# Optimization experiments

Measured on AMD Instinct MI355X. Metric: run time of the kernel, lower is better.

The kernel has to match this reference:

```python
import jax, jax.numpy as jnp
import numpy as np


def setup_inputs() -> dict:
    key = jax.random.key(0)
    ks = jax.random.split(key, 4)
    B, S, D, V = 2, 2048, 768, 50257
    scale = 1.0 / np.sqrt(D)
    x = jax.random.normal(ks[0], (B, S, D), dtype=jnp.float32)
    W_vocab = jax.random.normal(ks[1], (V, D), dtype=jnp.float32) * scale
    b_vocab = jnp.zeros((V,), dtype=jnp.float32)
    W_lin = jax.random.normal(ks[2], (D, D), dtype=jnp.float32) * scale
    b_lin = jnp.zeros((D,), dtype=jnp.float32)
    return {"x": x, "W_vocab": W_vocab, "b_vocab": b_vocab, "W_lin": W_lin, "b_lin": b_lin}


def reference(x, W_vocab, b_vocab, W_lin, b_lin):
    # vocab_attention_layer(x): [B,S,D] @ [D,V] + b -> [B,S,V]
    logits = jnp.einsum('bsd,vd->bsv', x, W_vocab) + b_vocab
    va = jax.nn.softmax(logits, axis=-1)                      # [B,S,V]
    # einsum('bij,jk->bik', va, weight): contract vocab against embedding rows
    va_weight = jnp.einsum('bsv,vd->bsd', va, W_vocab)        # [B,S,D]
    # final nn.Linear(d_model, d_model): y = h @ W^T + b
    return jnp.einsum('bsd,ed->bse', va_weight, W_lin) + b_lin
```

## Files before the change

### kernel.cpp

```cpp
#include <hip/hip_runtime.h>
#include <hip/hip_bf16.h>
#include <stdint.h>

typedef float f32x4 __attribute__((ext_vector_type(4)));
typedef short s16x8 __attribute__((ext_vector_type(8)));
typedef unsigned short u16;

#define M_ROWS 4096
#define DIM    768
#define VOCAB  50257
#define VP2    50432

#define OFF_XB     0ull
#define OFF_WLB    6291456ull
#define OFF_WVB    7471104ull
#define OFF_WVT    84934656ull
#define OFF_P      162398208ull
#define OFF_ORUN   229507072ull
#define OFF_LROW   242089984ull
#define OFF_BROW   242106368ull
#define OFF_KEYS   242122752ull
#define OFF_H      242122880ull

__device__ __forceinline__ u16 f2bf(float f) {
    union { float f; unsigned u; } x; x.f = f;
    return (u16)((x.u + 0x7fffu + ((x.u >> 16) & 1u)) >> 16);
}
__device__ __forceinline__ float bf2f_hi(unsigned u) {
    union { unsigned u; float f; } x; x.u = u & 0xffff0000u; return x.f;
}
__device__ __forceinline__ float bf2f_lo(unsigned u) {
    union { unsigned u; float f; } x; x.u = u << 16; return x.f;
}
__device__ __forceinline__ unsigned fkey(float f) {
    union { float f; unsigned u; } x; x.f = f;
    return (x.u & 0x80000000u) ? ~x.u : (x.u | 0x80000000u);
}
__device__ __forceinline__ float fkey_dec(unsigned k) {
    union { unsigned u; float f; } x;
    x.u = (k & 0x80000000u) ? (k & 0x7fffffffu) : ~k;
    return x.f;
}
__device__ __forceinline__ void glds16(const u16* g, u16* l) {
    __builtin_amdgcn_global_load_lds(
        (const __attribute__((address_space(1))) unsigned int*)g,
        (__attribute__((address_space(3))) unsigned int*)l,
        16, 0, 0);
}

__global__ __launch_bounds__(256) void cast_bf16(const float* __restrict__ src,
                                                 u16* __restrict__ dst, int n4) {
    int i = blockIdx.x * 256 + threadIdx.x;
    if (i >= n4) return;
    float4 v = ((const float4*)src)[i];
    ushort4 o;
    o.x = f2bf(v.x); o.y = f2bf(v.y); o.z = f2bf(v.z); o.w = f2bf(v.w);
    ((ushort4*)dst)[i] = o;
}

__global__ __launch_bounds__(256) void prep_wvb(const float* __restrict__ wv,
                                                u16* __restrict__ wvb, int ntask) {
    int t = blockIdx.x * 256 + threadIdx.x;
    if (t >= ntask) return;
    int v = t / 96, ch = t % 96;
    uint4 pk = {0u, 0u, 0u, 0u};
    if (v < VOCAB) {
        const float* p = wv + (size_t)v * DIM + ch * 8;
        float4 f0 = ((const float4*)p)[0];
        float4 f1 = ((const float4*)p)[1];
        pk.x = (unsigned)f2bf(f0.x) | ((unsigned)f2bf(f0.y) << 16);
        pk.y = (unsigned)f2bf(f0.z) | ((unsigned)f2bf(f0.w) << 16);
        pk.z = (unsigned)f2bf(f1.x) | ((unsigned)f2bf(f1.y) << 16);
        pk.w = (unsigned)f2bf(f1.z) | ((unsigned)f2bf(f1.w) << 16);
    }
    *(uint4*)(wvb + (size_t)v * DIM + ch * 8) = pk;
}

__global__ void init_keys(unsigned* keys) {
    keys[0] = 0u;
    keys[1] = fkey(-3.0e38f);
}

__global__ __launch_bounds__(256) void wnorm(const u16* __restrict__ wvb,
                                             unsigned* __restrict__ keys) {
    __shared__ float part[128];
    int tid = threadIdx.x;
    int vb = blockIdx.x * 32;
    int vl = tid & 31, cg = tid >> 5;
    float s = 0.f;
    #pragma unroll
    for (int it = 0; it < 12; ++it) {
        int ch = cg + 8 * it;
        uint4 pk = *(const uint4*)(wvb + (size_t)(vb + vl) * DIM + ch * 8);
        const unsigned* pw = (const unsigned*)&pk;
        #pragma unroll
        for (int k = 0; k < 4; ++k) {
            float lo = bf2f_lo(pw[k]), hi = bf2f_hi(pw[k]);
            s += lo * lo + hi * hi;
        }
    }
    s += __shfl_xor(s, 32);
    int w = tid >> 6, lane = tid & 63;
    if (lane < 32) part[w * 32 + lane] = s;
    __syncthreads();
    if (tid < 32) {
        float t = part[tid] + part[32 + tid] + part[64 + tid] + part[96 + tid];
        float n = sqrtf(t);
        #pragma unroll
        for (int msk = 1; msk < 32; msk <<= 1) n = fmaxf(n, __shfl_xor(n, msk));
        if (tid == 0) atomicMax(&keys[0], __float_as_uint(n));
    }
}

__global__ __launch_bounds__(256) void bmax_k(const float* __restrict__ bv,
                                              unsigned* __restrict__ keys) {
    int i = blockIdx.x * 256 + threadIdx.x;
    float v = (i < VOCAB) ? bv[i] : -3.0e38f;
    #pragma unroll
    for (int msk = 1; msk < 64; msk <<= 1) v = fmaxf(v, __shfl_xor(v, msk));
    if ((threadIdx.x & 63) == 0) atomicMax(&keys[1], fkey(v));
}

__global__ __launch_bounds__(256) void xnorm(const float* __restrict__ x,
                                             const unsigned* __restrict__ keys,
                                             float* __restrict__ Brow) {
    int w = threadIdx.x >> 6, lane = threadIdx.x & 63;
    int r = blockIdx.x * 4 + w;
    const float4* p = (const float4*)(x + (size_t)r * DIM);
    float s = 0.f;
    #pragma unroll
    for (int it = 0; it < 3; ++it) {
        float4 v = p[it * 64 + lane];
        s += v.x * v.x + v.y * v.y + v.z * v.z + v.w * v.w;
    }
    #pragma unroll
    for (int msk = 1; msk < 64; msk <<= 1) s += __shfl_xor(s, msk);
    if (lane == 0) {
        float Wn = __uint_as_float(keys[0]);
        float bm = fkey_dec(keys[1]);
        Brow[r] = sqrtf(s) * Wn * 1.01f + bm + 0.1f;
    }
}

__global__ __launch_bounds__(256) void prep_wvt(const u16* __restrict__ wvb,
                                                u16* __restrict__ wvt) {
    __shared__ u16 tile[32][776];
    int vb = blockIdx.x * 32;
    int tid = threadIdx.x;
    #pragma unroll
    for (int it = 0; it < 12; ++it) {
        int task = tid + 256 * it;
        int row = task / 96, ch = task % 96;
        *(uint4*)(&tile[row][ch * 8]) = *(const uint4*)(wvb + (size_t)(vb + row) * DIM + ch * 8);
    }
    __syncthreads();
    #pragma unroll
    for (int it = 0; it < 12; ++it) {
        int task = tid + 256 * it;
        int d = task >> 2, vg = task & 3;
        u16 t8[8];
        #pragma unroll
        for (int j = 0; j < 8; ++j) t8[j] = tile[vg * 8 + j][d];
        uint4 pk;
        pk.x = (unsigned)t8[0] | ((unsigned)t8[1] << 16);
        pk.y = (unsigned)t8[2] | ((unsigned)t8[3] << 16);
        pk.z = (unsigned)t8[4] | ((unsigned)t8[5] << 16);
        pk.w = (unsigned)t8[6] | ((unsigned)t8[7] << 16);
        *(uint4*)(wvt + (size_t)d * VP2 + vb + vg * 8) = pk;
    }
}


template<int MH, int NH>
__device__ __forceinline__ void mfma_quad(f32x4 (&acc)[8][4],
                                          const s16x8 (&afr)[4][2],
                                          const s16x8 (&bfr)[2][2][2]) {
    #pragma unroll
    for (int mi = 0; mi < 4; ++mi)
        #pragma unroll
        for (int ni = 0; ni < 2; ++ni) {
            f32x4 a_ = acc[MH * 4 + mi][NH * 2 + ni];
            a_ = __builtin_amdgcn_mfma_f32_16x16x32_bf16(afr[mi][0], bfr[NH][ni][0], a_, 0, 0, 0);
            a_ = __builtin_amdgcn_mfma_f32_16x16x32_bf16(afr[mi][1], bfr[NH][ni][1], a_, 0, 0, 0);
            acc[MH * 4 + mi][NH * 2 + ni] = a_;
        }
}

#define STG(g, pitch, rowbase, kcol, ldst) do {                                   \
    const u16* _s0 = (g) + (size_t)((rowbase) + rlo) * (pitch) + (kcol) + offu;   \
    const u16* _s1 = _s0 + (size_t)64 * (pitch);                                  \
    glds16(_s0, (u16*)(ldst) + (size_t)tid * 8);                                  \
    glds16(_s1, (u16*)(ldst) + (size_t)tid * 8 + 4096);                           \
} while (0)

#define RD_A(buf, mh) do { _Pragma("unroll")                                              \
    for (int _mi = 0; _mi < 4; ++_mi) {                                                   \
        afr[_mi][0] = *(const s16x8*)((buf) + ((abase + ((mh)*4 + _mi)*2048)      ^ asw));\
        afr[_mi][1] = *(const s16x8*)((buf) + ((abase + ((mh)*4 + _mi)*2048 + 64) ^ asw));\
    } } while (0)

#define RD_B(buf, nh) do { _Pragma("unroll")                                              \
    for (int _ni = 0; _ni < 2; ++_ni) {                                                   \
        bfr[nh][_ni][0] = *(const s16x8*)((buf) + ((bbase + ((nh)*2 + _ni)*2048)      ^ asw));\
        bfr[nh][_ni][1] = *(const s16x8*)((buf) + ((bbase + ((nh)*2 + _ni)*2048 + 64) ^ asw));\
    } } while (0)

#define PH_SYNC1() do { __builtin_amdgcn_s_barrier();                      \
    asm volatile("s_waitcnt lgkmcnt(0)" ::: "memory");                     \
    __builtin_amdgcn_s_setprio(1); } while (0)
#define PH_SYNC2() do { __builtin_amdgcn_s_setprio(0);                     \
    __builtin_amdgcn_s_barrier(); } while (0)

__device__ __forceinline__ void kloop256(char* LDS,
                                         const u16* __restrict__ gA, int pA,
                                         const u16* __restrict__ gB, int pB,
                                         int NT, int tid, f32x4 (&acc)[8][4]) {
    const int lane = tid & 63, w = tid >> 6;
    const int c = lane & 15, q = (lane >> 4) & 3;
    const int wm = w & 1, wn = w >> 1;
    const int asw = (c & 7) << 4;
    const int abase = wm * 16384 + c * 128 + q * 16;
    const int bbase = (wn >> 1) * 16384 + (wn & 1) * 8192 + c * 128 + q * 16;
    const int rlo = tid >> 3;
    const int offu = ((tid & 7) * 8) ^ ((rlo & 7) << 3);
    char* A0 = LDS;
    char* B0 = LDS + 32768;
    char* A1 = LDS + 65536;
    char* B1 = LDS + 98304;
    s16x8 afr[4][2], bfr[2][2][2];
    const int ktN = NT - 1;

    STG(gA, pA, 0,   0, A0);
    STG(gA, pA, 128, 0, A0 + 16384);
    STG(gB, pB, 0,   0, B0);
    STG(gB, pB, 128, 0, B0 + 16384);
    {
        int k1 = (ktN >= 1 ? 1 : 0) * 64;
        STG(gB, pB, 0,   k1, B1);
        STG(gB, pB, 128, k1, B1 + 16384);
        STG(gA, pA, 0,   k1, A1);
    }
    asm volatile("s_waitcnt vmcnt(6)" ::: "memory");
    __builtin_amdgcn_s_barrier();

    const int nit = NT >> 1;
    #pragma unroll 1
    for (int it2 = 0; it2 < nit; ++it2) {
        int kO  = ((2 * it2 + 1 < NT) ? 2 * it2 + 1 : ktN) * 64;
        int kN0 = ((2 * it2 + 2 < NT) ? 2 * it2 + 2 : ktN) * 64;
        int kN1 = ((2 * it2 + 3 < NT) ? 2 * it2 + 3 : ktN) * 64;
        RD_A(A0, 0); RD_B(B0, 0);
        STG(gA, pA, 128, kO, A1 + 16384);
        PH_SYNC1(); mfma_quad<0, 0>(acc, afr, bfr); PH_SYNC2();
        RD_B(B0, 1);
        PH_SYNC1(); mfma_quad<0, 1>(acc, afr, bfr); PH_SYNC2();
        RD_A(A0, 1);
        STG(gB, pB, 0, kN0, B0);
        PH_SYNC1(); mfma_quad<1, 0>(acc, afr, bfr); PH_SYNC2();
        STG(gB, pB, 128, kN0, B0 + 16384);
        STG(gA, pA, 0,   kN0, A0);
        asm volatile("s_waitcnt vmcnt(6)" ::: "memory");
        PH_SYNC1(); mfma_quad<1, 1>(acc, afr, bfr); PH_SYNC2();
        RD_A(A1, 0); RD_B(B1, 0);
        STG(gA, pA, 128, kN0, A0 + 16384);
        PH_SYNC1(); mfma_quad<0, 0>(acc, afr, bfr); PH_SYNC2();
        RD_B(B1, 1);
        PH_SYNC1(); mfma_quad<0, 1>(acc, afr, bfr); PH_SYNC2();
        RD_A(A1, 1);
        STG(gB, pB, 0, kN1, B1);
        PH_SYNC1(); mfma_quad<1, 0>(acc, afr, bfr); PH_SYNC2();
        STG(gB, pB, 128, kN1, B1 + 16384);
        STG(gA, pA, 0,   kN1, A1);
        asm volatile("s_waitcnt vmcnt(6)" ::: "memory");
        PH_SYNC1(); mfma_quad<1, 1>(acc, afr, bfr); PH_SYNC2();
    }
}

__global__ __launch_bounds__(512, 2) void gemm1(
    const u16* __restrict__ xb, const u16* __restrict__ wvb,
    const float* __restrict__ bvocab, const float* __restrict__ Brow,
    u16* __restrict__ P, float* __restrict__ Lrow, int v0, int CN) {
    __shared__ __align__(16) char LDS[131072];
    __shared__ float BL[256];
    int tid = threadIdx.x;
    int mt = blockIdx.x & 15, nt = blockIdx.x >> 4;
    if (tid < 256) BL[tid] = Brow[mt * 256 + tid];
    f32x4 acc[8][4];
    #pragma unroll
    for (int i = 0; i < 8; ++i)
        #pragma unroll
        for (int j = 0; j < 4; ++j) acc[i][j] = (f32x4){0.f, 0.f, 0.f, 0.f};
    kloop256(LDS, xb + (size_t)(mt * 256) * DIM, DIM,
             wvb + (size_t)(v0 + nt * 256) * DIM, DIM, 12, tid, acc);

    int lane = tid & 63, w = tid >> 6, c = lane & 15, q = (lane >> 4) & 3;
    int wm = w & 1, wn = w >> 1;
    float bvv[4]; bool vok[4];
    #pragma unroll
    for (int n = 0; n < 4; ++n) {
        int vg = v0 + nt * 256 + wn * 64 + n * 16 + c;
        vok[n] = vg < VOCAB;
        bvv[n] = vok[n] ? bvocab[vg] : 0.f;
    }
    #pragma unroll
    for (int m = 0; m < 8; ++m)
        #pragma unroll
        for (int jr = 0; jr < 4; ++jr) {
            int rloc = wm * 128 + m * 16 + q * 4 + jr;
            float B = BL[rloc];
            float s = 0.f;
            #pragma unroll
            for (int n = 0; n < 4; ++n) {
                float z = acc[m][n][jr] + bvv[n];
                float e = vok[n] ? __expf(z - B) : 0.f;
                acc[m][n][jr] = e;
                s += e;
            }
            s += __shfl_xor(s, 1); s += __shfl_xor(s, 2);
            s += __shfl_xor(s, 4); s += __shfl_xor(s, 8);
            if (c == 0) atomicAdd(&Lrow[mt * 256 + rloc], s);
        }
    u16* Pt = (u16*)LDS;
    #pragma unroll
    for (int h = 0; h < 2; ++h) {
        if (h) __syncthreads();
        if (wm == h) {
            #pragma unroll
            for (int m = 0; m < 8; ++m)
                #pragma unroll
                for (int jr = 0; jr < 4; ++jr) {
                    int r = m * 16 + q * 4 + jr;
                    #pragma unroll
                    for (int n = 0; n < 4; ++n)
                        Pt[r * 256 + wn * 64 + n * 16 + c] = f2bf(acc[m][n][jr]);
                }
        }
        __syncthreads();
        #pragma unroll
        for (int itc = 0; itc < 8; ++itc) {
            int task = tid + itc * 512;
            int r = task >> 5, chn = task & 31;
            uint4 pk = *(const uint4*)(Pt + r * 256 + chn * 8);
            *(uint4*)(P + (size_t)(mt * 256 + h * 128 + r) * CN + nt * 256 + chn * 8) = pk;
        }
    }
}

__global__ __launch_bounds__(512, 2) void gemm2(
    const u16* __restrict__ P, const u16* __restrict__ wvt,
    float* __restrict__ Orun, int CN, int v0, int KT) {
    __shared__ __align__(16) char LDS[131072];
    int tid = threadIdx.x;
    int mt = blockIdx.x & 15;
    int rest = blockIdx.x >> 4;
    int nt = rest % 3, s = rest / 3;
    int ks0 = ((KT + 9) / 10) * 2;
    int k0 = s * ks0;
    if (k0 >= KT) return;
    int NTs = (k0 + ks0 <= KT) ? ks0 : (KT - k0);
    f32x4 acc[8][4];
    #pragma unroll
    for (int i = 0; i < 8; ++i)
        #pragma unroll
        for (int j = 0; j < 4; ++j) acc[i][j] = (f32x4){0.f, 0.f, 0.f, 0.f};
    kloop256(LDS, P + (size_t)(mt * 256) * CN + k0 * 64, CN,
             wvt + (size_t)(nt * 256) * VP2 + v0 + k0 * 64, VP2, NTs, tid, acc);

    int lane = tid & 63, w = tid >> 6, c = lane & 15, q = (lane >> 4) & 3;
    int wm = w & 1, wn = w >> 1;
    #pragma unroll
    for (int m = 0; m < 8; ++m)
        #pragma unroll
        for (int n = 0; n < 4; ++n) {
            int col = nt * 256 + wn * 64 + n * 16 + c;
            #pragma unroll
            for (int jr = 0; jr < 4; ++jr) {
                int row = mt * 256 + wm * 128 + m * 16 + q * 4 + jr;
                atomicAdd(&Orun[(size_t)row * DIM + col], acc[m][n][jr]);
            }
        }
}

__global__ __launch_bounds__(256) void final_h(const float* __restrict__ Orun,
                                               const float* __restrict__ Lrow,
                                               u16* __restrict__ h) {
    int idx = blockIdx.x * 256 + threadIdx.x;
    if (idx >= M_ROWS * DIM) return;
    int r = idx / DIM;
    h[idx] = f2bf(Orun[idx] / Lrow[r]);
}

__global__ __launch_bounds__(256, 2) void final_gemm(const u16* __restrict__ h,
                                                     const u16* __restrict__ wlb,
                                                     const float* __restrict__ blin,
                                                     float* __restrict__ out) {
    __shared__ u16 At[4096];
    __shared__ u16 Bt[4096];
    int mb = blockIdx.x & 31, eb = blockIdx.x >> 5;
    int tid = threadIdx.x;
    int w = tid >> 6, lane = tid & 63, q = lane >> 4, c = lane & 15;
    int wm = w & 1, wn = w >> 1;
    int trow = tid >> 2, tch = tid & 3;
    const u16* gA0 = h + (size_t)(mb * 128 + trow) * DIM + tch * 8;
    const u16* gA1 = h + (size_t)(mb * 128 + 64 + trow) * DIM + tch * 8;
    const u16* gB0 = wlb + (size_t)(eb * 128 + trow) * DIM + tch * 8;
    const u16* gB1 = wlb + (size_t)(eb * 128 + 64 + trow) * DIM + tch * 8;
    f32x4 acc[4][4];
    #pragma unroll
    for (int i = 0; i < 4; ++i)
        #pragma unroll
        for (int j = 0; j < 4; ++j) acc[i][j] = (f32x4){0.f, 0.f, 0.f, 0.f};

    for (int ko = 0; ko < 24; ++ko) {
        glds16(gA0 + ko * 32, At + tid * 8);
        glds16(gA1 + ko * 32, At + (tid + 256) * 8);
        glds16(gB0 + ko * 32, Bt + tid * 8);
        glds16(gB1 + ko * 32, Bt + (tid + 256) * 8);
        __syncthreads();
        s16x8 af[4], bf[4];
        #pragma unroll
        for (int i = 0; i < 4; ++i)
            af[i] = *(const s16x8*)(At + (wm * 64 + i * 16 + c) * 32 + q * 8);
        #pragma unroll
        for (int j = 0; j < 4; ++j)
            bf[j] = *(const s16x8*)(Bt + (wn * 64 + j * 16 + c) * 32 + q * 8);
        #pragma unroll
        for (int i = 0; i < 4; ++i)
            #pragma unroll
            for (int j = 0; j < 4; ++j)
                acc[i][j] = __builtin_amdgcn_mfma_f32_16x16x32_bf16(af[i], bf[j], acc[i][j], 0, 0, 0);
        __syncthreads();
    }
    #pragma unroll
    for (int j = 0; j < 4; ++j) {
        int e = eb * 128 + wn * 64 + j * 16 + c;
        float bl = blin[e];
        #pragma unroll
        for (int i = 0; i < 4; ++i) {
            #pragma unroll
            for (int jr = 0; jr < 4; ++jr) {
                int row = mb * 128 + wm * 64 + i * 16 + q * 4 + jr;
                out[(size_t)row * DIM + e] = acc[i][j][jr] + bl;
            }
        }
    }
}

extern "C" void kernel_launch(void* const* d_in, const int* in_sizes, int n_in,
                              void* d_out, int out_size, void* d_ws, size_t ws_size,
                              hipStream_t stream) {
    const float* x  = (const float*)d_in[0];
    const float* Wv = (const float*)d_in[1];
    const float* bv = (const float*)d_in[2];
    const float* Wl = (const float*)d_in[3];
    const float* bl = (const float*)d_in[4];
    float* out = (float*)d_out;
    char* ws = (char*)d_ws;

    u16* xb   = (u16*)(ws + OFF_XB);
    u16* wlb  = (u16*)(ws + OFF_WLB);
    u16* wvb  = (u16*)(ws + OFF_WVB);
    u16* wvt  = (u16*)(ws + OFF_WVT);
    u16* P    = (u16*)(ws + OFF_P);
    float* Orun  = (float*)(ws + OFF_ORUN);
    float* Lrow  = (float*)(ws + OFF_LROW);
    float* Brow  = (float*)(ws + OFF_BROW);
    unsigned* keys = (unsigned*)(ws + OFF_KEYS);
    u16* h       = (u16*)(ws + OFF_H);

    cast_bf16<<<(M_ROWS * DIM / 4 + 255) / 256, 256, 0, stream>>>(x, xb, M_ROWS * DIM / 4);
    cast_bf16<<<(DIM * DIM / 4 + 255) / 256, 256, 0, stream>>>(Wl, wlb, DIM * DIM / 4);
    {
        int ntask = VP2 * 96;
        prep_wvb<<<(ntask + 255) / 256, 256, 0, stream>>>(Wv, wvb, ntask);
    }
    init_keys<<<1, 1, 0, stream>>>(keys);
    hipMemsetAsync(Orun, 0, (size_t)M_ROWS * DIM * 4, stream);
    hipMemsetAsync(Lrow, 0, (size_t)M_ROWS * 4, stream);
    wnorm<<<VP2 / 32, 256, 0, stream>>>(wvb, keys);
    bmax_k<<<(VOCAB + 255) / 256, 256, 0, stream>>>(bv, keys);
    xnorm<<<M_ROWS / 4, 256, 0, stream>>>(x, keys, Brow);
    prep_wvt<<<VP2 / 32, 256, 0, stream>>>(wvb, wvt);

    static const int chunk_start[7] = {0, 32, 64, 96, 128, 160, 192};
    static const int chunk_cnt[7]   = {32, 32, 32, 32, 32, 32, 5};
    for (int ci = 0; ci < 7; ++ci) {
        int cnt = chunk_cnt[ci];
        int v0 = chunk_start[ci] * 256;
        int CN = cnt * 256;
        int KT = CN / 64;
        gemm1<<<16 * cnt, 512, 0, stream>>>(xb, wvb, bv, Brow, P, Lrow, v0, CN);
        gemm2<<<240, 512, 0, stream>>>(P, wvt, Orun, CN, v0, KT);
    }
    final_h<<<(M_ROWS * DIM + 255) / 256, 256, 0, stream>>>(Orun, Lrow, h);
    final_gemm<<<192, 256, 0, stream>>>(h, wlb, bl, out);
}
```

Before: 1.414 ms.

## Restructure GEMM k-loop pipeline, pre-tile transposed vocab weights, swizzle workgroups across XCDs

Rewrites the shared double-buffered k-loop so it uses fewer barriers per iteration, with explicit vmcnt/lgkmcnt waits and sched barriers, and merges MFMA quads into larger phases. The transposed vocab weight is stored as contiguous 64x256 tiles, so gemm2's B loads read one contiguous block per k-step instead of rows strided by VP2. Both GEMMs remap block IDs so neighbouring tiles are spread across the 8 XCDs for better L2 locality. The risks are races from the reduced synchronisation and changed load ordering between the LDS buffers.

```diff
diff --git a/kernel.cpp b/kernel.cpp
--- a/kernel.cpp
+++ b/kernel.cpp
@@ -10,6 +10,7 @@
 #define DIM    768
 #define VOCAB  50257
 #define VP2    50432
+#define KTOT   788
 
 #define OFF_XB     0ull
 #define OFF_WLB    6291456ull
@@ -142,10 +143,12 @@
     }
 }
 
-__global__ __launch_bounds__(256) void prep_wvt(const u16* __restrict__ wvb,
-                                                u16* __restrict__ wvt) {
+__global__ __launch_bounds__(256) void prep_wvtb(const u16* __restrict__ wvb,
+                                                 u16* __restrict__ wvtb) {
     __shared__ u16 tile[32][776];
     int vb = blockIdx.x * 32;
+    int kt = vb >> 6;
+    int vhalf = (vb >> 5) & 1;
     int tid = threadIdx.x;
     #pragma unroll
     for (int it = 0; it < 12; ++it) {
@@ -157,16 +160,17 @@
     #pragma unroll
     for (int it = 0; it < 12; ++it) {
         int task = tid + 256 * it;
-        int d = task >> 2, vg = task & 3;
+        int nt = task >> 10, rem = task & 1023;
+        int dd = rem >> 2, vg = rem & 3;
         u16 t8[8];
         #pragma unroll
-        for (int j = 0; j < 8; ++j) t8[j] = tile[vg * 8 + j][d];
+        for (int j = 0; j < 8; ++j) t8[j] = tile[vg * 8 + j][nt * 256 + dd];
         uint4 pk;
         pk.x = (unsigned)t8[0] | ((unsigned)t8[1] << 16);
         pk.y = (unsigned)t8[2] | ((unsigned)t8[3] << 16);
         pk.z = (unsigned)t8[4] | ((unsigned)t8[5] << 16);
         pk.w = (unsigned)t8[6] | ((unsigned)t8[7] << 16);
-        *(uint4*)(wvt + (size_t)d * VP2 + vb + vg * 8) = pk;
+        *(uint4*)(wvtb + (size_t)(nt * KTOT + kt) * 16384 + dd * 64 + vhalf * 32 + vg * 8) = pk;
     }
 }
 
@@ -205,15 +209,17 @@
         bfr[nh][_ni][1] = *(const s16x8*)((buf) + ((bbase + ((nh)*2 + _ni)*2048 + 64) ^ asw));\
     } } while (0)
 
-#define PH_SYNC1() do { __builtin_amdgcn_s_barrier();                      \
-    asm volatile("s_waitcnt lgkmcnt(0)" ::: "memory");                     \
-    __builtin_amdgcn_s_setprio(1); } while (0)
-#define PH_SYNC2() do { __builtin_amdgcn_s_setprio(0);                     \
-    __builtin_amdgcn_s_barrier(); } while (0)
+#define SP1() __builtin_amdgcn_s_setprio(1)
+#define SP0() __builtin_amdgcn_s_setprio(0)
+#define BARRIER() __builtin_amdgcn_s_barrier()
+#define WAIT_VM4() do { asm volatile("s_waitcnt vmcnt(4)" ::: "memory"); \
+    __builtin_amdgcn_sched_barrier(0); } while (0)
+#define WAIT_LGKM0() do { asm volatile("s_waitcnt lgkmcnt(0)" ::: "memory"); \
+    __builtin_amdgcn_sched_barrier(0); } while (0)
 
 __device__ __forceinline__ void kloop256(char* LDS,
                                          const u16* __restrict__ gA, int pA,
-                                         const u16* __restrict__ gB, int pB,
+                                         const u16* __restrict__ gB, int pB, int ksB,
                                          int NT, int tid, f32x4 (&acc)[8][4]) {
     const int lane = tid & 63, w = tid >> 6;
     const int c = lane & 15, q = (lane >> 4) & 3;
@@ -235,44 +241,47 @@
     STG(gB, pB, 0,   0, B0);
     STG(gB, pB, 128, 0, B0 + 16384);
     {
-        int k1 = (ktN >= 1 ? 1 : 0) * 64;
-        STG(gB, pB, 0,   k1, B1);
-        STG(gB, pB, 128, k1, B1 + 16384);
-        STG(gA, pA, 0,   k1, A1);
-    }
-    asm volatile("s_waitcnt vmcnt(6)" ::: "memory");
-    __builtin_amdgcn_s_barrier();
+        int t1 = (1 <= ktN) ? 1 : ktN;
+        STG(gB, pB, 0,   t1 * ksB, B1);
+        STG(gB, pB, 128, t1 * ksB, B1 + 16384);
+    }
+    WAIT_VM4();
+    BARRIER();
 
     const int nit = NT >> 1;
     #pragma unroll 1
     for (int it2 = 0; it2 < nit; ++it2) {
-        int kO  = ((2 * it2 + 1 < NT) ? 2 * it2 + 1 : ktN) * 64;
-        int kN0 = ((2 * it2 + 2 < NT) ? 2 * it2 + 2 : ktN) * 64;
-        int kN1 = ((2 * it2 + 3 < NT) ? 2 * it2 + 3 : ktN) * 64;
-        RD_A(A0, 0); RD_B(B0, 0);
-        STG(gA, pA, 128, kO, A1 + 16384);
-        PH_SYNC1(); mfma_quad<0, 0>(acc, afr, bfr); PH_SYNC2();
-        RD_B(B0, 1);
-        PH_SYNC1(); mfma_quad<0, 1>(acc, afr, bfr); PH_SYNC2();
+        int t1 = (2 * it2 + 1 <= ktN) ? 2 * it2 + 1 : ktN;
+        int t2 = (2 * it2 + 2 <= ktN) ? 2 * it2 + 2 : ktN;
+        int t3 = (2 * it2 + 3 <= ktN) ? 2 * it2 + 3 : ktN;
+        RD_A(A0, 0); RD_B(B0, 0); RD_B(B0, 1);
+        STG(gA, pA, 0,   t1 * 64, A1);
+        STG(gA, pA, 128, t1 * 64, A1 + 16384);
+        SP1(); mfma_quad<0, 0>(acc, afr, bfr); SP0();
+        WAIT_LGKM0();
+        BARRIER();
+        STG(gB, pB, 0,   t2 * ksB, B0);
+        STG(gB, pB, 128, t2 * ksB, B0 + 16384);
+        SP1(); mfma_quad<0, 1>(acc, afr, bfr); SP0();
         RD_A(A0, 1);
-        STG(gB, pB, 0, kN0, B0);
-        PH_SYNC1(); mfma_quad<1, 0>(acc, afr, bfr); PH_SYNC2();
-        STG(gB, pB, 128, kN0, B0 + 16384);
-        STG(gA, pA, 0,   kN0, A0);
-        asm volatile("s_waitcnt vmcnt(6)" ::: "memory");
-        PH_SYNC1(); mfma_quad<1, 1>(acc, afr, bfr); PH_SYNC2();
-        RD_A(A1, 0); RD_B(B1, 0);
-        STG(gA, pA, 128, kN0, A0 + 16384);
-        PH_SYNC1(); mfma_quad<0, 0>(acc, afr, bfr); PH_SYNC2();
-        RD_B(B1, 1);
-        PH_SYNC1(); mfma_quad<0, 1>(acc, afr, bfr); PH_SYNC2();
+        SP1(); mfma_quad<1, 0>(acc, afr, bfr);
+               mfma_quad<1, 1>(acc, afr, bfr); SP0();
+        WAIT_VM4();
+        BARRIER();
+        RD_A(A1, 0); RD_B(B1, 0); RD_B(B1, 1);
+        STG(gA, pA, 0,   t2 * 64, A0);
+        STG(gA, pA, 128, t2 * 64, A0 + 16384);
+        SP1(); mfma_quad<0, 0>(acc, afr, bfr); SP0();
+        WAIT_LGKM0();
+        BARRIER();
+        STG(gB, pB, 0,   t3 * ksB, B1);
+        STG(gB, pB, 128, t3 * ksB, B1 + 16384);
+        SP1(); mfma_quad<0, 1>(acc, afr, bfr); SP0();
         RD_A(A1, 1);
-        STG(gB, pB, 0, kN1, B1);
-        PH_SYNC1(); mfma_quad<1, 0>(acc, afr, bfr); PH_SYNC2();
-        STG(gB, pB, 128, kN1, B1 + 16384);
-        STG(gA, pA, 0,   kN1, A1);
-        asm volatile("s_waitcnt vmcnt(6)" ::: "memory");
-        PH_SYNC1(); mfma_quad<1, 1>(acc, afr, bfr); PH_SYNC2();
+        SP1(); mfma_quad<1, 0>(acc, afr, bfr);
+               mfma_quad<1, 1>(acc, afr, bfr); SP0();
+        WAIT_VM4();
+        BARRIER();
     }
 }
 
@@ -283,7 +292,10 @@
     __shared__ __align__(16) char LDS[131072];
     __shared__ float BL[256];
     int tid = threadIdx.x;
-    int mt = blockIdx.x & 15, nt = blockIdx.x >> 4;
+    int nwg = gridDim.x, cpx = nwg >> 3;
+    int bid = blockIdx.x;
+    bid = (bid & 7) * cpx + (bid >> 3);
+    int mt = bid & 15, nt = bid >> 4;
     if (tid < 256) BL[tid] = Brow[mt * 256 + tid];
     f32x4 acc[8][4];
     #pragma unroll
@@ -291,7 +303,7 @@
         #pragma unroll
         for (int j = 0; j < 4; ++j) acc[i][j] = (f32x4){0.f, 0.f, 0.f, 0.f};
     kloop256(LDS, xb + (size_t)(mt * 256) * DIM, DIM,
-             wvb + (size_t)(v0 + nt * 256) * DIM, DIM, 12, tid, acc);
+             wvb + (size_t)(v0 + nt * 256) * DIM, DIM, 64, 12, tid, acc);
 
     int lane = tid & 63, w = tid >> 6, c = lane & 15, q = (lane >> 4) & 3;
     int wm = w & 1, wn = w >> 1;
@@ -347,12 +359,15 @@
 }
 
 __global__ __launch_bounds__(512, 2) void gemm2(
-    const u16* __restrict__ P, const u16* __restrict__ wvt,
+    const u16* __restrict__ P, const u16* __restrict__ wvtb,
     float* __restrict__ Orun, int CN, int v0, int KT) {
     __shared__ __align__(16) char LDS[131072];
     int tid = threadIdx.x;
-    int mt = blockIdx.x & 15;
-    int rest = blockIdx.x >> 4;
+    int nwg = gridDim.x, cpx = nwg >> 3;
+    int bid = blockIdx.x;
+    bid = (bid & 7) * cpx + (bid >> 3);
+    int mt = bid & 15;
+    int rest = bid >> 4;
     int nt = rest % 3, s = rest / 3;
     int ks0 = ((KT + 9) / 10) * 2;
     int k0 = s * ks0;
@@ -364,7 +379,8 @@
         #pragma unroll
         for (int j = 0; j < 4; ++j) acc[i][j] = (f32x4){0.f, 0.f, 0.f, 0.f};
     kloop256(LDS, P + (size_t)(mt * 256) * CN + k0 * 64, CN,
-             wvt + (size_t)(nt * 256) * VP2 + v0 + k0 * 64, VP2, NTs, tid, acc);
+             wvtb + (size_t)(nt * KTOT + (v0 >> 6) + k0) * 16384, 64, 16384,
+             NTs, tid, acc);
 
     int lane = tid & 63, w = tid >> 6, c = lane & 15, q = (lane >> 4) & 3;
     int wm = w & 1, wn = w >> 1;
@@ -460,7 +476,7 @@
     u16* xb   = (u16*)(ws + OFF_XB);
     u16* wlb  = (u16*)(ws + OFF_WLB);
     u16* wvb  = (u16*)(ws + OFF_WVB);
-    u16* wvt  = (u16*)(ws + OFF_WVT);
+    u16* wvtb = (u16*)(ws + OFF_WVT);
     u16* P    = (u16*)(ws + OFF_P);
     float* Orun  = (float*)(ws + OFF_ORUN);
     float* Lrow  = (float*)(ws + OFF_LROW);
@@ -480,7 +496,7 @@
     wnorm<<<VP2 / 32, 256, 0, stream>>>(wvb, keys);
     bmax_k<<<(VOCAB + 255) / 256, 256, 0, stream>>>(bv, keys);
     xnorm<<<M_ROWS / 4, 256, 0, stream>>>(x, keys, Brow);
-    prep_wvt<<<VP2 / 32, 256, 0, stream>>>(wvb, wvt);
+    prep_wvtb<<<VP2 / 32, 256, 0, stream>>>(wvb, wvtb);
 
     static const int chunk_start[7] = {0, 32, 64, 96, 128, 160, 192};
     static const int chunk_cnt[7]   = {32, 32, 32, 32, 32, 32, 5};
@@ -490,7 +506,7 @@
         int CN = cnt * 256;
         int KT = CN / 64;
         gemm1<<<16 * cnt, 512, 0, stream>>>(xb, wvb, bv, Brow, P, Lrow, v0, CN);
-        gemm2<<<240, 512, 0, stream>>>(P, wvt, Orun, CN, v0, KT);
+        gemm2<<<240, 512, 0, stream>>>(P, wvtb, Orun, CN, v0, KT);
     }
     final_h<<<(M_ROWS * DIM + 255) / 256, 256, 0, stream>>>(Orun, Lrow, h);
     final_gemm<<<192, 256, 0, stream>>>(h, wlb, bl, out);
```

Result: faster. 1.363 ms (-3.6%).

## Rewrite vocab GEMMs with 1024-thread blocks, K=32 triple-buffered loop and tiled WvT layout

Applied to the files above, without the earlier changes.

Replaces the 512-thread, 256x256 tile, K=64 double-buffered phased main loop with a simpler 1024-thread, 16-wave loop that stages K=32 slices through three LDS buffers using an XOR swizzle. The transposed vocab weight is re-laid out as contiguous 32-row K-tiles so gemm2 reads dense blocks, and both GEMMs remap block IDs across 8 groups, with gemm2 split into 6 K-slices over 288 blocks. The goal is higher wave occupancy, lower LDS use and more coalesced loads. In exchange it drops the fine-grained MFMA/load interleaving and priority scheduling, adds more barriers per unit of K, and gemm2 does more atomic adds because K is split more finely.

```diff
diff --git a/kernel.cpp b/kernel.cpp
--- a/kernel.cpp
+++ b/kernel.cpp
@@ -10,6 +10,7 @@
 #define DIM    768
 #define VOCAB  50257
 #define VP2    50432
+#define KT32   1576
 
 #define OFF_XB     0ull
 #define OFF_WLB    6291456ull
@@ -142,10 +143,11 @@
     }
 }
 
-__global__ __launch_bounds__(256) void prep_wvt(const u16* __restrict__ wvb,
-                                                u16* __restrict__ wvt) {
+__global__ __launch_bounds__(256) void prep_wvt32(const u16* __restrict__ wvb,
+                                                  u16* __restrict__ wvt32) {
     __shared__ u16 tile[32][776];
-    int vb = blockIdx.x * 32;
+    int kt = blockIdx.x;
+    int vb = kt * 32;
     int tid = threadIdx.x;
     #pragma unroll
     for (int it = 0; it < 12; ++it) {
@@ -166,135 +168,88 @@
         pk.y = (unsigned)t8[2] | ((unsigned)t8[3] << 16);
         pk.z = (unsigned)t8[4] | ((unsigned)t8[5] << 16);
         pk.w = (unsigned)t8[6] | ((unsigned)t8[7] << 16);
-        *(uint4*)(wvt + (size_t)d * VP2 + vb + vg * 8) = pk;
-    }
-}
-
-
-template<int MH, int NH>
-__device__ __forceinline__ void mfma_quad(f32x4 (&acc)[8][4],
-                                          const s16x8 (&afr)[4][2],
-                                          const s16x8 (&bfr)[2][2][2]) {
-    #pragma unroll
-    for (int mi = 0; mi < 4; ++mi)
-        #pragma unroll
-        for (int ni = 0; ni < 2; ++ni) {
-            f32x4 a_ = acc[MH * 4 + mi][NH * 2 + ni];
-            a_ = __builtin_amdgcn_mfma_f32_16x16x32_bf16(afr[mi][0], bfr[NH][ni][0], a_, 0, 0, 0);
-            a_ = __builtin_amdgcn_mfma_f32_16x16x32_bf16(afr[mi][1], bfr[NH][ni][1], a_, 0, 0, 0);
-            acc[MH * 4 + mi][NH * 2 + ni] = a_;
-        }
-}
-
-#define STG(g, pitch, rowbase, kcol, ldst) do {                                   \
-    const u16* _s0 = (g) + (size_t)((rowbase) + rlo) * (pitch) + (kcol) + offu;   \
-    const u16* _s1 = _s0 + (size_t)64 * (pitch);                                  \
-    glds16(_s0, (u16*)(ldst) + (size_t)tid * 8);                                  \
-    glds16(_s1, (u16*)(ldst) + (size_t)tid * 8 + 4096);                           \
-} while (0)
-
-#define RD_A(buf, mh) do { _Pragma("unroll")                                              \
-    for (int _mi = 0; _mi < 4; ++_mi) {                                                   \
-        afr[_mi][0] = *(const s16x8*)((buf) + ((abase + ((mh)*4 + _mi)*2048)      ^ asw));\
-        afr[_mi][1] = *(const s16x8*)((buf) + ((abase + ((mh)*4 + _mi)*2048 + 64) ^ asw));\
-    } } while (0)
-
-#define RD_B(buf, nh) do { _Pragma("unroll")                                              \
-    for (int _ni = 0; _ni < 2; ++_ni) {                                                   \
-        bfr[nh][_ni][0] = *(const s16x8*)((buf) + ((bbase + ((nh)*2 + _ni)*2048)      ^ asw));\
-        bfr[nh][_ni][1] = *(const s16x8*)((buf) + ((bbase + ((nh)*2 + _ni)*2048 + 64) ^ asw));\
-    } } while (0)
-
-#define PH_SYNC1() do { __builtin_amdgcn_s_barrier();                      \
-    asm volatile("s_waitcnt lgkmcnt(0)" ::: "memory");                     \
-    __builtin_amdgcn_s_setprio(1); } while (0)
-#define PH_SYNC2() do { __builtin_amdgcn_s_setprio(0);                     \
-    __builtin_amdgcn_s_barrier(); } while (0)
-
-__device__ __forceinline__ void kloop256(char* LDS,
-                                         const u16* __restrict__ gA, int pA,
-                                         const u16* __restrict__ gB, int pB,
-                                         int NT, int tid, f32x4 (&acc)[8][4]) {
+        *(uint4*)(wvt32 + (size_t)kt * 24576 + d * 32 + vg * 8) = pk;
+    }
+}
+
+__device__ __forceinline__ void kloop2(char* LDS,
+                                       const u16* __restrict__ gA, size_t sA,
+                                       const u16* __restrict__ gB, size_t sB,
+                                       int nk, int tid, f32x4 (&acc)[4][4]) {
     const int lane = tid & 63, w = tid >> 6;
     const int c = lane & 15, q = (lane >> 4) & 3;
-    const int wm = w & 1, wn = w >> 1;
-    const int asw = (c & 7) << 4;
-    const int abase = wm * 16384 + c * 128 + q * 16;
-    const int bbase = (wn >> 1) * 16384 + (wn & 1) * 8192 + c * 128 + q * 16;
-    const int rlo = tid >> 3;
-    const int offu = ((tid & 7) * 8) ^ ((rlo & 7) << 3);
-    char* A0 = LDS;
-    char* B0 = LDS + 32768;
-    char* A1 = LDS + 65536;
-    char* B1 = LDS + 98304;
-    s16x8 afr[4][2], bfr[2][2][2];
-    const int ktN = NT - 1;
-
-    STG(gA, pA, 0,   0, A0);
-    STG(gA, pA, 128, 0, A0 + 16384);
-    STG(gB, pB, 0,   0, B0);
-    STG(gB, pB, 128, 0, B0 + 16384);
+    const int wm = w & 3, wn = w >> 2;
+    const int xsw = (q ^ (c & 3)) * 16;
+    char* p0 = LDS;
+    char* p1 = LDS + 32768;
+    char* p2 = LDS + 65536;
+
+    glds16(gA, (u16*)(p0 + (size_t)tid * 16));
+    glds16(gB, (u16*)(p0 + 16384 + (size_t)tid * 16));
     {
-        int k1 = (ktN >= 1 ? 1 : 0) * 64;
-        STG(gB, pB, 0,   k1, B1);
-        STG(gB, pB, 128, k1, B1 + 16384);
-        STG(gA, pA, 0,   k1, A1);
-    }
-    asm volatile("s_waitcnt vmcnt(6)" ::: "memory");
+        size_t t1 = (nk > 1) ? 1 : 0;
+        glds16(gA + t1 * sA, (u16*)(p1 + (size_t)tid * 16));
+        glds16(gB + t1 * sB, (u16*)(p1 + 16384 + (size_t)tid * 16));
+    }
+    asm volatile("s_waitcnt vmcnt(2)" ::: "memory");
+    __builtin_amdgcn_sched_barrier(0);
     __builtin_amdgcn_s_barrier();
-
-    const int nit = NT >> 1;
+    __builtin_amdgcn_sched_barrier(0);
+
     #pragma unroll 1
-    for (int it2 = 0; it2 < nit; ++it2) {
-        int kO  = ((2 * it2 + 1 < NT) ? 2 * it2 + 1 : ktN) * 64;
-        int kN0 = ((2 * it2 + 2 < NT) ? 2 * it2 + 2 : ktN) * 64;
-        int kN1 = ((2 * it2 + 3 < NT) ? 2 * it2 + 3 : ktN) * 64;
-        RD_A(A0, 0); RD_B(B0, 0);
-        STG(gA, pA, 128, kO, A1 + 16384);
-        PH_SYNC1(); mfma_quad<0, 0>(acc, afr, bfr); PH_SYNC2();
-        RD_B(B0, 1);
-        PH_SYNC1(); mfma_quad<0, 1>(acc, afr, bfr); PH_SYNC2();
-        RD_A(A0, 1);
-        STG(gB, pB, 0, kN0, B0);
-        PH_SYNC1(); mfma_quad<1, 0>(acc, afr, bfr); PH_SYNC2();
-        STG(gB, pB, 128, kN0, B0 + 16384);
-        STG(gA, pA, 0,   kN0, A0);
-        asm volatile("s_waitcnt vmcnt(6)" ::: "memory");
-        PH_SYNC1(); mfma_quad<1, 1>(acc, afr, bfr); PH_SYNC2();
-        RD_A(A1, 0); RD_B(B1, 0);
-        STG(gA, pA, 128, kN0, A0 + 16384);
-        PH_SYNC1(); mfma_quad<0, 0>(acc, afr, bfr); PH_SYNC2();
-        RD_B(B1, 1);
-        PH_SYNC1(); mfma_quad<0, 1>(acc, afr, bfr); PH_SYNC2();
-        RD_A(A1, 1);
-        STG(gB, pB, 0, kN1, B1);
-        PH_SYNC1(); mfma_quad<1, 0>(acc, afr, bfr); PH_SYNC2();
-        STG(gB, pB, 128, kN1, B1 + 16384);
-        STG(gA, pA, 0,   kN1, A1);
-        asm volatile("s_waitcnt vmcnt(6)" ::: "memory");
-        PH_SYNC1(); mfma_quad<1, 1>(acc, afr, bfr); PH_SYNC2();
-    }
-}
-
-__global__ __launch_bounds__(512, 2) void gemm1(
+    for (int t = 0; t < nk; ++t) {
+        size_t t2 = (size_t)((t + 2 < nk) ? (t + 2) : (nk - 1));
+        glds16(gA + t2 * sA, (u16*)(p2 + (size_t)tid * 16));
+        glds16(gB + t2 * sB, (u16*)(p2 + 16384 + (size_t)tid * 16));
+        s16x8 af[4], bf[4];
+        #pragma unroll
+        for (int i = 0; i < 4; ++i)
+            af[i] = *(const s16x8*)(p0 + (wm * 64 + i * 16 + c) * 64 + xsw);
+        #pragma unroll
+        for (int j = 0; j < 4; ++j)
+            bf[j] = *(const s16x8*)(p0 + 16384 + (wn * 64 + j * 16 + c) * 64 + xsw);
+        #pragma unroll
+        for (int i = 0; i < 4; ++i)
+            #pragma unroll
+            for (int j = 0; j < 4; ++j)
+                acc[i][j] = __builtin_amdgcn_mfma_f32_16x16x32_bf16(af[i], bf[j], acc[i][j], 0, 0, 0);
+        asm volatile("s_waitcnt vmcnt(2)" ::: "memory");
+        __builtin_amdgcn_sched_barrier(0);
+        __builtin_amdgcn_s_barrier();
+        __builtin_amdgcn_sched_barrier(0);
+        char* tp = p0; p0 = p1; p1 = p2; p2 = tp;
+    }
+    asm volatile("s_waitcnt vmcnt(0)" ::: "memory");
+    __builtin_amdgcn_sched_barrier(0);
+    __builtin_amdgcn_s_barrier();
+}
+
+__global__ __launch_bounds__(1024, 4) void gemm1(
     const u16* __restrict__ xb, const u16* __restrict__ wvb,
     const float* __restrict__ bvocab, const float* __restrict__ Brow,
     u16* __restrict__ P, float* __restrict__ Lrow, int v0, int CN) {
-    __shared__ __align__(16) char LDS[131072];
+    __shared__ __align__(16) char LDS[98304];
     __shared__ float BL[256];
     int tid = threadIdx.x;
-    int mt = blockIdx.x & 15, nt = blockIdx.x >> 4;
+    int nwg = gridDim.x, cpx = nwg >> 3;
+    int bid = blockIdx.x;
+    bid = (bid & 7) * cpx + (bid >> 3);
+    int mt = bid & 15, nt = bid >> 4;
     if (tid < 256) BL[tid] = Brow[mt * 256 + tid];
-    f32x4 acc[8][4];
-    #pragma unroll
-    for (int i = 0; i < 8; ++i)
+    f32x4 acc[4][4];
+    #pragma unroll
+    for (int i = 0; i < 4; ++i)
         #pragma unroll
         for (int j = 0; j < 4; ++j) acc[i][j] = (f32x4){0.f, 0.f, 0.f, 0.f};
-    kloop256(LDS, xb + (size_t)(mt * 256) * DIM, DIM,
-             wvb + (size_t)(v0 + nt * 256) * DIM, DIM, 12, tid, acc);
+
+    int row = tid >> 2;
+    int qg = (tid & 3) ^ (row & 3);
+    const u16* gA = xb + (size_t)(mt * 256 + row) * DIM + qg * 8;
+    const u16* gB = wvb + (size_t)(v0 + nt * 256 + row) * DIM + qg * 8;
+    kloop2(LDS, gA, 32, gB, 32, 24, tid, acc);
 
     int lane = tid & 63, w = tid >> 6, c = lane & 15, q = (lane >> 4) & 3;
-    int wm = w & 1, wn = w >> 1;
+    int wm = w & 3, wn = w >> 2;
     float bvv[4]; bool vok[4];
     #pragma unroll
     for (int n = 0; n < 4; ++n) {
@@ -303,17 +258,17 @@
         bvv[n] = vok[n] ? bvocab[vg] : 0.f;
     }
     #pragma unroll
-    for (int m = 0; m < 8; ++m)
+    for (int i = 0; i < 4; ++i)
         #pragma unroll
         for (int jr = 0; jr < 4; ++jr) {
-            int rloc = wm * 128 + m * 16 + q * 4 + jr;
+            int rloc = wm * 64 + i * 16 + q * 4 + jr;
             float B = BL[rloc];
             float s = 0.f;
             #pragma unroll
             for (int n = 0; n < 4; ++n) {
-                float z = acc[m][n][jr] + bvv[n];
+                float z = acc[i][n][jr] + bvv[n];
                 float e = vok[n] ? __expf(z - B) : 0.f;
-                acc[m][n][jr] = e;
+                acc[i][n][jr] = e;
                 s += e;
             }
             s += __shfl_xor(s, 1); s += __shfl_xor(s, 2);
@@ -324,21 +279,21 @@
     #pragma unroll
     for (int h = 0; h < 2; ++h) {
         if (h) __syncthreads();
-        if (wm == h) {
-            #pragma unroll
-            for (int m = 0; m < 8; ++m)
+        if ((wm >> 1) == h) {
+            #pragma unroll
+            for (int i = 0; i < 4; ++i)
                 #pragma unroll
                 for (int jr = 0; jr < 4; ++jr) {
-                    int r = m * 16 + q * 4 + jr;
+                    int r = (wm & 1) * 64 + i * 16 + q * 4 + jr;
                     #pragma unroll
                     for (int n = 0; n < 4; ++n)
-                        Pt[r * 256 + wn * 64 + n * 16 + c] = f2bf(acc[m][n][jr]);
+                        Pt[r * 256 + wn * 64 + n * 16 + c] = f2bf(acc[i][n][jr]);
                 }
         }
         __syncthreads();
         #pragma unroll
-        for (int itc = 0; itc < 8; ++itc) {
-            int task = tid + itc * 512;
+        for (int itc = 0; itc < 4; ++itc) {
+            int task = tid + itc * 1024;
             int r = task >> 5, chn = task & 31;
             uint4 pk = *(const uint4*)(Pt + r * 256 + chn * 8);
             *(uint4*)(P + (size_t)(mt * 256 + h * 128 + r) * CN + nt * 256 + chn * 8) = pk;
@@ -346,37 +301,42 @@
     }
 }
 
-__global__ __launch_bounds__(512, 2) void gemm2(
-    const u16* __restrict__ P, const u16* __restrict__ wvt,
+__global__ __launch_bounds__(1024, 4) void gemm2(
+    const u16* __restrict__ P, const u16* __restrict__ wvt32,
     float* __restrict__ Orun, int CN, int v0, int KT) {
-    __shared__ __align__(16) char LDS[131072];
+    __shared__ __align__(16) char LDS[98304];
     int tid = threadIdx.x;
-    int mt = blockIdx.x & 15;
-    int rest = blockIdx.x >> 4;
-    int nt = rest % 3, s = rest / 3;
-    int ks0 = ((KT + 9) / 10) * 2;
+    int bid = (blockIdx.x & 7) * 36 + (blockIdx.x >> 3);
+    int s = bid / 48;
+    int rem = bid % 48;
+    int nd = rem >> 4, mt = rem & 15;
+    int ks0 = (KT + 5) / 6;
     int k0 = s * ks0;
     if (k0 >= KT) return;
-    int NTs = (k0 + ks0 <= KT) ? ks0 : (KT - k0);
-    f32x4 acc[8][4];
-    #pragma unroll
-    for (int i = 0; i < 8; ++i)
+    int nk = (k0 + ks0 <= KT) ? ks0 : (KT - k0);
+    f32x4 acc[4][4];
+    #pragma unroll
+    for (int i = 0; i < 4; ++i)
         #pragma unroll
         for (int j = 0; j < 4; ++j) acc[i][j] = (f32x4){0.f, 0.f, 0.f, 0.f};
-    kloop256(LDS, P + (size_t)(mt * 256) * CN + k0 * 64, CN,
-             wvt + (size_t)(nt * 256) * VP2 + v0 + k0 * 64, VP2, NTs, tid, acc);
+
+    int row = tid >> 2;
+    int qg = (tid & 3) ^ (row & 3);
+    const u16* gA = P + (size_t)(mt * 256 + row) * CN + (size_t)k0 * 32 + qg * 8;
+    const u16* gB = wvt32 + (size_t)((v0 >> 5) + k0) * 24576 + (size_t)(nd * 256 + row) * 32 + qg * 8;
+    kloop2(LDS, gA, 32, gB, 24576, nk, tid, acc);
 
     int lane = tid & 63, w = tid >> 6, c = lane & 15, q = (lane >> 4) & 3;
-    int wm = w & 1, wn = w >> 1;
-    #pragma unroll
-    for (int m = 0; m < 8; ++m)
+    int wm = w & 3, wn = w >> 2;
+    #pragma unroll
+    for (int i = 0; i < 4; ++i)
         #pragma unroll
         for (int n = 0; n < 4; ++n) {
-            int col = nt * 256 + wn * 64 + n * 16 + c;
+            int col = nd * 256 + wn * 64 + n * 16 + c;
             #pragma unroll
             for (int jr = 0; jr < 4; ++jr) {
-                int row = mt * 256 + wm * 128 + m * 16 + q * 4 + jr;
-                atomicAdd(&Orun[(size_t)row * DIM + col], acc[m][n][jr]);
+                int rg = mt * 256 + wm * 64 + i * 16 + q * 4 + jr;
+                atomicAdd(&Orun[(size_t)rg * DIM + col], acc[i][n][jr]);
             }
         }
 }
@@ -439,8 +399,8 @@
         for (int i = 0; i < 4; ++i) {
             #pragma unroll
             for (int jr = 0; jr < 4; ++jr) {
-                int row = mb * 128 + wm * 64 + i * 16 + q * 4 + jr;
-                out[(size_t)row * DIM + e] = acc[i][j][jr] + bl;
+                int rg = mb * 128 + wm * 64 + i * 16 + q * 4 + jr;
+                out[(size_t)rg * DIM + e] = acc[i][j][jr] + bl;
             }
         }
     }
@@ -457,11 +417,11 @@
     float* out = (float*)d_out;
     char* ws = (char*)d_ws;
 
-    u16* xb   = (u16*)(ws + OFF_XB);
-    u16* wlb  = (u16*)(ws + OFF_WLB);
-    u16* wvb  = (u16*)(ws + OFF_WVB);
-    u16* wvt  = (u16*)(ws + OFF_WVT);
-    u16* P    = (u16*)(ws + OFF_P);
+    u16* xb    = (u16*)(ws + OFF_XB);
+    u16* wlb   = (u16*)(ws + OFF_WLB);
+    u16* wvb   = (u16*)(ws + OFF_WVB);
+    u16* wvt32 = (u16*)(ws + OFF_WVT);
+    u16* P     = (u16*)(ws + OFF_P);
     float* Orun  = (float*)(ws + OFF_ORUN);
     float* Lrow  = (float*)(ws + OFF_LROW);
     float* Brow  = (float*)(ws + OFF_BROW);
@@ -480,7 +440,7 @@
     wnorm<<<VP2 / 32, 256, 0, stream>>>(wvb, keys);
     bmax_k<<<(VOCAB + 255) / 256, 256, 0, stream>>>(bv, keys);
     xnorm<<<M_ROWS / 4, 256, 0, stream>>>(x, keys, Brow);
-    prep_wvt<<<VP2 / 32, 256, 0, stream>>>(wvb, wvt);
+    prep_wvt32<<<KT32, 256, 0, stream>>>(wvb, wvt32);
 
     static const int chunk_start[7] = {0, 32, 64, 96, 128, 160, 192};
     static const int chunk_cnt[7]   = {32, 32, 32, 32, 32, 32, 5};
@@ -488,9 +448,9 @@
         int cnt = chunk_cnt[ci];
         int v0 = chunk_start[ci] * 256;
         int CN = cnt * 256;
-        int KT = CN / 64;
-        gemm1<<<16 * cnt, 512, 0, stream>>>(xb, wvb, bv, Brow, P, Lrow, v0, CN);
-        gemm2<<<240, 512, 0, stream>>>(P, wvt, Orun, CN, v0, KT);
+        int KT = CN / 32;
+        gemm1<<<16 * cnt, 1024, 0, stream>>>(xb, wvb, bv, Brow, P, Lrow, v0, CN);
+        gemm2<<<288, 1024, 0, stream>>>(P, wvt32, Orun, CN, v0, KT);
     }
     final_h<<<(M_ROWS * DIM + 255) / 256, 256, 0, stream>>>(Orun, Lrow, h);
     final_gemm<<<192, 256, 0, stream>>>(h, wlb, bl, out);
```

Measured after the change: 1.647 ms. 16.4% more time.
